# Performance work log

Hardware: AMD Instinct MI355X
Metric: run time of the kernel (lower is better)

Reference implementation:

```python
import jax, jax.numpy as jnp
import numpy as np

N, E, G = 20000, 320000, 32


def setup_inputs() -> dict:
    key = jax.random.key(0)
    ks = list(jax.random.split(key, 16))
    def nrm(i, shape, s):
        return jax.random.normal(ks[i], shape, jnp.float32) * s
    inp = {}
    inp['x'] = nrm(0, (N, 768), 1.0)
    inp['edge_index'] = jax.random.randint(ks[1], (2, E), 0, N)
    inp['batch'] = jnp.sort(jax.random.randint(ks[2], (N,), 0, G))
    # xavier-ish scales
    inp['proj_w'] = nrm(3, (768, 768), 0.036); inp['proj_b'] = jnp.zeros((768,), jnp.float32)
    inp['gat1_w'] = nrm(4, (768, 1024), 0.033)
    inp['att1_src'] = nrm(5, (4, 256), 0.06); inp['att1_dst'] = nrm(6, (4, 256), 0.06)
    inp['gat1_b'] = jnp.zeros((1024,), jnp.float32)
    inp['ln1_g'] = jnp.ones((1024,), jnp.float32); inp['ln1_b'] = jnp.zeros((1024,), jnp.float32)
    inp['gat2_w'] = nrm(7, (1024, 1024), 0.031)
    inp['att2_src'] = nrm(8, (4, 256), 0.06); inp['att2_dst'] = nrm(9, (4, 256), 0.06)
    inp['gat2_b'] = jnp.zeros((1024,), jnp.float32)
    inp['ln2_g'] = jnp.ones((1024,), jnp.float32); inp['ln2_b'] = jnp.zeros((1024,), jnp.float32)
    inp['gat3_w'] = nrm(10, (1024, 256), 0.04)
    inp['att3_src'] = nrm(11, (1, 256), 0.08); inp['att3_dst'] = nrm(12, (1, 256), 0.08)
    inp['gat3_b'] = jnp.zeros((256,), jnp.float32)
    inp['ln3_g'] = jnp.ones((256,), jnp.float32); inp['ln3_b'] = jnp.zeros((256,), jnp.float32)
    inp['cls1_w'] = nrm(13, (768, 128), 0.047); inp['cls1_b'] = jnp.zeros((128,), jnp.float32)
    inp['cls2_w'] = nrm(14, (128, 1), 0.12); inp['cls2_b'] = jnp.zeros((1,), jnp.float32)
    return inp


def layer_norm(x, g, b, eps=1e-5):
    mu = x.mean(-1, keepdims=True)
    v = ((x - mu) ** 2).mean(-1, keepdims=True)
    return (x - mu) * jax.lax.rsqrt(v + eps) * g + b


def gat_conv(x, src, dst, W, a_src, a_dst, bias, concat):
    # PyG GATConv (eval mode): linear -> per-head additive attention ->
    # segment softmax over incoming edges of each dst node -> scatter-sum.
    n = x.shape[0]
    H, C = a_src.shape
    h = (x @ W).reshape(n, H, C)                      # [N,H,C]
    e_s = (h * a_src[None]).sum(-1)                   # [N,H]
    e_d = (h * a_dst[None]).sum(-1)                   # [N,H]
    logits = jax.nn.leaky_relu(e_s[src] + e_d[dst], 0.2)   # [Etot,H]
    m = jax.ops.segment_max(logits, dst, num_segments=n)   # self-loops -> no empty segments
    ex = jnp.exp(logits - m[dst])
    den = jax.ops.segment_sum(ex, dst, num_segments=n)
    alpha = ex / (den[dst] + 1e-16)                   # [Etot,H]
    out = jax.ops.segment_sum(h[src] * alpha[:, :, None], dst, num_segments=n)  # [N,H,C]
    out = out.reshape(n, H * C) if concat else out.mean(axis=1)
    return out + bias


def reference(x, edge_index, batch, proj_w, proj_b,
              gat1_w, att1_src, att1_dst, gat1_b, ln1_g, ln1_b,
              gat2_w, att2_src, att2_dst, gat2_b, ln2_g, ln2_b,
              gat3_w, att3_src, att3_dst, gat3_b, ln3_g, ln3_b,
              cls1_w, cls1_b, cls2_w, cls2_b):
    n = x.shape[0]
    loop = jnp.arange(n)
    src = jnp.concatenate([edge_index[0], loop])  # GATConv adds self-loops
    dst = jnp.concatenate([edge_index[1], loop])
    h = jax.nn.elu(x @ proj_w + proj_b)
    x1 = jax.nn.elu(layer_norm(gat_conv(h, src, dst, gat1_w, att1_src, att1_dst, gat1_b, True), ln1_g, ln1_b))
    x2 = jax.nn.elu(layer_norm(gat_conv(x1, src, dst, gat2_w, att2_src, att2_dst, gat2_b, True), ln2_g, ln2_b)) + x1
    x3 = jax.nn.elu(layer_norm(gat_conv(x2, src, dst, gat3_w, att3_src, att3_dst, gat3_b, False), ln3_g, ln3_b))
    cnt = jax.ops.segment_sum(jnp.ones((n, 1), x3.dtype), batch, num_segments=G)
    s = jax.ops.segment_sum(x3, batch, num_segments=G)
    mean = s / jnp.maximum(cnt, 1.0)
    mx = jax.ops.segment_max(x3, batch, num_segments=G)
    pooled = jnp.concatenate([mean, mx, s], axis=1)   # [G, 3*256]
    out = jax.nn.relu(pooled @ cls1_w + cls1_b) @ cls2_w + cls2_b
    return out.reshape(-1)
```

## Files before the change

### kernel.cpp

```cpp
#include <hip/hip_runtime.h>
#include <math.h>

typedef float floatx4 __attribute__((ext_vector_type(4)));
typedef _Float16 f16x8 __attribute__((ext_vector_type(8)));
typedef _Float16 f16x4 __attribute__((ext_vector_type(4)));

template<int N> struct f16vec_t;
template<> struct f16vec_t<4> { typedef f16x4 type; };
template<> struct f16vec_t<8> { typedef f16x8 type; };

__device__ __forceinline__ unsigned encf(float f) {
    unsigned u = __float_as_uint(f);
    return (u & 0x80000000u) ? ~u : (u | 0x80000000u);
}
__device__ __forceinline__ float decf(unsigned u) {
    u = (u & 0x80000000u) ? (u & 0x7FFFFFFFu) : ~u;
    return __uint_as_float(u);
}
__device__ __forceinline__ void glds16(const void* g, void* l) {
    __builtin_amdgcn_global_load_lds(
        (const __attribute__((address_space(1))) unsigned int*)g,
        (__attribute__((address_space(3))) unsigned int*)l, 16, 0, 0);
}

__global__ __launch_bounds__(256) void cvt_f16_kernel(
    const float* __restrict__ in, _Float16* __restrict__ out, size_t n4)
{
    size_t i = (size_t)blockIdx.x * 256 + threadIdx.x;
    if (i >= n4) return;
    float4 v = ((const float4*)in)[i];
    f16x4 o;
    o[0] = (_Float16)v.x; o[1] = (_Float16)v.y; o[2] = (_Float16)v.z; o[3] = (_Float16)v.w;
    ((f16x4*)out)[i] = o;
}

__global__ __launch_bounds__(256) void wt_kernel(
    const float* __restrict__ w, _Float16* __restrict__ wt, int K, int N)
{
    __shared__ float t[32][33];
    int bx = blockIdx.x * 32, by = blockIdx.y * 32;
    int tx = threadIdx.x & 31, ty = threadIdx.x >> 5;
    for (int r = ty; r < 32; r += 8)
        t[r][tx] = w[(size_t)(by + r) * N + bx + tx];
    __syncthreads();
    for (int r = ty; r < 32; r += 8)
        wt[(size_t)(bx + r) * K + by + tx] = (_Float16)t[tx][r];
}

__global__ __launch_bounds__(256) void gemm_f16(
    const _Float16* __restrict__ A, const _Float16* __restrict__ BT,
    const float* __restrict__ bias, _Float16* __restrict__ C,
    int M, int K, int N, int act)
{
    __shared__ _Float16 Al[2][128 * 32];
    __shared__ _Float16 Bl[2][128 * 32];
    int tid = threadIdx.x;
    int lane = tid & 63, wave = tid >> 6;
    int row0 = blockIdx.y * 128, col0 = blockIdx.x * 128;
    int wm = (wave >> 1) * 64, wn = (wave & 1) * 64;
    int l15 = lane & 15, quad = lane >> 4;

    int rg0 = wave * 2, rg1 = rg0 + 1;
    int srow0 = rg0 * 16 + (lane >> 2);
    int srow1 = rg1 * 16 + (lane >> 2);
    int scol = (lane & 3) * 8;
    int arow0 = row0 + srow0; if (arow0 > M - 1) arow0 = M - 1;
    int arow1 = row0 + srow1; if (arow1 > M - 1) arow1 = M - 1;
    const _Float16* gA0 = A + (size_t)arow0 * K + scol;
    const _Float16* gA1 = A + (size_t)arow1 * K + scol;
    const _Float16* gB0 = BT + (size_t)(col0 + srow0) * K + scol;
    const _Float16* gB1 = BT + (size_t)(col0 + srow1) * K + scol;

    floatx4 acc[4][4] = {};

    glds16(gA0, &Al[0][rg0 * 512]);
    glds16(gA1, &Al[0][rg1 * 512]);
    glds16(gB0, &Bl[0][rg0 * 512]);
    glds16(gB1, &Bl[0][rg1 * 512]);

    int nk = K >> 5;
    for (int it = 0; it < nk; it++) {
        int cur = it & 1, nxt = cur ^ 1;
        __syncthreads();
        if (it + 1 < nk) {
            int k1 = (it + 1) << 5;
            glds16(gA0 + k1, &Al[nxt][rg0 * 512]);
            glds16(gA1 + k1, &Al[nxt][rg1 * 512]);
            glds16(gB0 + k1, &Bl[nxt][rg0 * 512]);
            glds16(gB1 + k1, &Bl[nxt][rg1 * 512]);
        }
        f16x8 af[4], bfr[4];
        #pragma unroll
        for (int i = 0; i < 4; i++) {
            af[i]  = *(const f16x8*)&Al[cur][(wm + i * 16 + l15) * 32 + quad * 8];
            bfr[i] = *(const f16x8*)&Bl[cur][(wn + i * 16 + l15) * 32 + quad * 8];
        }
        #pragma unroll
        for (int i = 0; i < 4; i++)
            #pragma unroll
            for (int j = 0; j < 4; j++)
                acc[i][j] = __builtin_amdgcn_mfma_f32_16x16x32_f16(af[i], bfr[j], acc[i][j], 0, 0, 0);
    }

    #pragma unroll
    for (int i = 0; i < 4; i++) {
        #pragma unroll
        for (int v = 0; v < 4; v++) {
            int gr = row0 + wm + i * 16 + quad * 4 + v;
            if (gr >= M) continue;
            #pragma unroll
            for (int j = 0; j < 4; j++) {
                int gc = col0 + wn + j * 16 + l15;
                float val = acc[i][j][v];
                if (bias) val += bias[gc];
                if (act) val = val > 0.f ? val : (expf(val) - 1.f);
                C[(size_t)gr * N + gc] = (_Float16)val;
            }
        }
    }
}

__global__ __launch_bounds__(256) void attn_scores_kernel(
    const _Float16* __restrict__ h, const float* __restrict__ asrc, const float* __restrict__ adst,
    float* __restrict__ es, float* __restrict__ ed, int Nn, int H)
{
    int wid = (blockIdx.x * 256 + threadIdx.x) >> 6;
    int lane = threadIdx.x & 63;
    if (wid >= Nn * H) return;
    int node = wid / H, hh = wid % H;
    const _Float16* hp = h + (size_t)node * H * 256 + hh * 256 + lane * 4;
    f16x4 v = *(const f16x4*)hp;
    float ss = 0.f, sd = 0.f;
    #pragma unroll
    for (int j = 0; j < 4; j++) {
        float f = (float)v[j];
        ss = fmaf(f, asrc[hh * 256 + lane * 4 + j], ss);
        sd = fmaf(f, adst[hh * 256 + lane * 4 + j], sd);
    }
    #pragma unroll
    for (int o = 32; o; o >>= 1) { ss += __shfl_down(ss, o); sd += __shfl_down(sd, o); }
    if (lane == 0) { es[wid] = ss; ed[wid] = sd; }
}

__global__ __launch_bounds__(256) void csr_init(int* __restrict__ deg, int Nn) {
    int i = blockIdx.x * 256 + threadIdx.x;
    if (i < Nn) deg[i] = 1;
}
__global__ __launch_bounds__(256) void csr_count(const int* __restrict__ ei, int* __restrict__ deg, int E) {
    int i = blockIdx.x * 256 + threadIdx.x;
    if (i < E) atomicAdd(&deg[ei[E + i]], 1);
}
__global__ __launch_bounds__(256) void scan1(const int* __restrict__ deg, int* __restrict__ incl,
                                             int* __restrict__ bsums, int Nn) {
    __shared__ int sd[256];
    int idx = blockIdx.x * 256 + threadIdx.x;
    sd[threadIdx.x] = (idx < Nn) ? deg[idx] : 0;
    __syncthreads();
    for (int o = 1; o < 256; o <<= 1) {
        int x = (threadIdx.x >= (unsigned)o) ? sd[threadIdx.x - o] : 0;
        __syncthreads();
        sd[threadIdx.x] += x;
        __syncthreads();
    }
    if (idx < Nn) incl[idx] = sd[threadIdx.x];
    if (threadIdx.x == 255) bsums[blockIdx.x] = sd[255];
}
__global__ void scan2(int* __restrict__ bsums, int nb) {
    if (blockIdx.x == 0 && threadIdx.x == 0) {
        int run = 0;
        for (int i = 0; i < nb; i++) { int v = bsums[i]; bsums[i] = run; run += v; }
    }
}
__global__ __launch_bounds__(256) void scan3(const int* __restrict__ incl, const int* __restrict__ deg,
                                             const int* __restrict__ bsums, int* __restrict__ rowstart,
                                             int* __restrict__ cursor, int Nn) {
    int idx = blockIdx.x * 256 + threadIdx.x;
    if (idx >= Nn) return;
    int rs = incl[idx] - deg[idx] + bsums[blockIdx.x];
    rowstart[idx] = rs;
    cursor[idx] = rs;
}
__global__ __launch_bounds__(256) void csr_fill(const int* __restrict__ ei, int* __restrict__ cursor,
                                                int* __restrict__ csrc, int E, int Nn) {
    int i = blockIdx.x * 256 + threadIdx.x;
    if (i >= E + Nn) return;
    int s, d;
    if (i < E) { s = ei[i]; d = ei[E + i]; } else { s = d = i - E; }
    int pos = atomicAdd(&cursor[d], 1);
    csrc[pos] = s;
}

template<int H>
__global__ __launch_bounds__(256) void seg_softmax(
    const int* __restrict__ rowstart, const int* __restrict__ deg,
    const int* __restrict__ csrc, const float* __restrict__ es,
    const float* __restrict__ ed, float* __restrict__ wse, int Nn)
{
    int d = (blockIdx.x * 256 + threadIdx.x) >> 6;
    int lane = threadIdx.x & 63;
    if (d >= Nn) return;
    constexpr int S = 64 / H;
    int head = lane & (H - 1);
    int slot = lane / H;
    int st = rowstart[d], dg = deg[d];
    float edv = ed[d * H + head];
    float m = -1e30f;
    for (int j = slot; j < dg; j += S) {
        float l = es[csrc[st + j] * H + head] + edv;
        l = l > 0.f ? l : 0.2f * l;
        wse[(size_t)(st + j) * H + head] = l;
        m = fmaxf(m, l);
    }
    #pragma unroll
    for (int o = H; o < 64; o <<= 1) m = fmaxf(m, __shfl_xor(m, o));
    float z = 0.f;
    for (int j = slot; j < dg; j += S) {
        float e = expf(wse[(size_t)(st + j) * H + head] - m);
        wse[(size_t)(st + j) * H + head] = e;
        z += e;
    }
    #pragma unroll
    for (int o = H; o < 64; o <<= 1) z += __shfl_xor(z, o);
    float rz = 1.f / (z + 1e-16f);
    for (int j = slot; j < dg; j += S)
        wse[(size_t)(st + j) * H + head] *= rz;
}

template<int H>
__global__ __launch_bounds__(H == 4 ? 128 : 64) void gat_gather_ln(
    const int* __restrict__ rowstart, const int* __restrict__ deg,
    const int* __restrict__ csrc, const float* __restrict__ wse,
    const _Float16* __restrict__ h,
    const float* __restrict__ bias, const float* __restrict__ gam,
    const float* __restrict__ bet, const float* resid,
    float* xout, _Float16* xout16)
{
    constexpr int T = (H == 4) ? 128 : 64;
    constexpr int CPT = (H == 4) ? 8 : 4;
    constexpr int NW = T / 64;
    constexpr int HC = H * 256;
    typedef typename f16vec_t<CPT>::type hvec;
    int d = blockIdx.x;
    int t = threadIdx.x;
    int lane = t & 63, wave = t >> 6;
    int ch0 = t * CPT;
    int head2 = ch0 >> 8;
    int st = rowstart[d], dg = deg[d];
    const _Float16* hb = h + ch0;

    float acc[CPT];
    #pragma unroll
    for (int k = 0; k < CPT; k++) acc[k] = 0.f;

    int j = 0;
    for (; j + 2 <= dg; j += 2) {
        int s0 = csrc[st + j], s1 = csrc[st + j + 1];
        float w0 = wse[(size_t)(st + j) * H + head2];
        float w1 = wse[(size_t)(st + j + 1) * H + head2];
        hvec v0 = *(const hvec*)(hb + (size_t)s0 * HC);
        hvec v1 = *(const hvec*)(hb + (size_t)s1 * HC);
        #pragma unroll
        for (int k = 0; k < CPT; k++)
            acc[k] += w0 * (float)v0[k] + w1 * (float)v1[k];
    }
    if (j < dg) {
        int s0 = csrc[st + j];
        float w0 = wse[(size_t)(st + j) * H + head2];
        hvec v0 = *(const hvec*)(hb + (size_t)s0 * HC);
        #pragma unroll
        for (int k = 0; k < CPT; k++) acc[k] += w0 * (float)v0[k];
    }

    #pragma unroll
    for (int k = 0; k < CPT; k++) acc[k] += bias[ch0 + k];

    __shared__ float sm[NW > 1 ? NW : 1];
    float sum = 0.f;
    #pragma unroll
    for (int k = 0; k < CPT; k++) sum += acc[k];
    #pragma unroll
    for (int o = 32; o; o >>= 1) sum += __shfl_down(sum, o);
    float tot;
    if (NW > 1) {
        if (lane == 0) sm[wave] = sum;
        __syncthreads();
        tot = 0.f;
        #pragma unroll
        for (int w2 = 0; w2 < NW; w2++) tot += sm[w2];
    } else {
        tot = __shfl(sum, 0);
    }
    float mean = tot / (float)HC;
    float sq = 0.f;
    #pragma unroll
    for (int k = 0; k < CPT; k++) { float dd = acc[k] - mean; sq = fmaf(dd, dd, sq); }
    #pragma unroll
    for (int o = 32; o; o >>= 1) sq += __shfl_down(sq, o);
    if (NW > 1) {
        __syncthreads();
        if (lane == 0) sm[wave] = sq;
        __syncthreads();
        tot = 0.f;
        #pragma unroll
        for (int w2 = 0; w2 < NW; w2++) tot += sm[w2];
    } else {
        tot = __shfl(sq, 0);
    }
    float rstd = rsqrtf(tot / (float)HC + 1e-5f);

    float y[CPT];
    #pragma unroll
    for (int k = 0; k < CPT; k++) {
        float v = (acc[k] - mean) * rstd * gam[ch0 + k] + bet[ch0 + k];
        y[k] = v > 0.f ? v : (expf(v) - 1.f);
    }
    if (resid) {
        #pragma unroll
        for (int q = 0; q < CPT / 4; q++) {
            float4 r = ((const float4*)resid)[(size_t)d * (HC / 4) + t * (CPT / 4) + q];
            y[q * 4 + 0] += r.x; y[q * 4 + 1] += r.y; y[q * 4 + 2] += r.z; y[q * 4 + 3] += r.w;
        }
    }
    #pragma unroll
    for (int q = 0; q < CPT / 4; q++)
        ((float4*)xout)[(size_t)d * (HC / 4) + t * (CPT / 4) + q] =
            make_float4(y[q * 4 + 0], y[q * 4 + 1], y[q * 4 + 2], y[q * 4 + 3]);
    if (xout16) {
        hvec o;
        #pragma unroll
        for (int k = 0; k < CPT; k++) o[k] = (_Float16)y[k];
        *(hvec*)(xout16 + (size_t)d * HC + ch0) = o;
    }
}

__global__ __launch_bounds__(256) void pool_kernel(
    const float* __restrict__ x3, const int* __restrict__ batch,
    float* __restrict__ ps, unsigned* __restrict__ pm, int* __restrict__ cnt, int Nn)
{
    int c = threadIdx.x;
    int n0 = blockIdx.x * 16;
    int end = n0 + 16; if (end > Nn) end = Nn;
    if (n0 >= Nn) return;
    int curg = batch[n0];
    float s = 0.f, m = -1e30f; int k = 0;
    for (int n = n0; n < end; n++) {
        int g = batch[n];
        if (g != curg) {
            atomicAdd(&ps[curg * 256 + c], s);
            atomicMax(&pm[curg * 256 + c], encf(m));
            if (c == 0) atomicAdd(&cnt[curg], k);
            s = 0.f; m = -1e30f; k = 0; curg = g;
        }
        float v = x3[(size_t)n * 256 + c];
        s += v; m = fmaxf(m, v); k++;
    }
    atomicAdd(&ps[curg * 256 + c], s);
    atomicMax(&pm[curg * 256 + c], encf(m));
    if (c == 0) atomicAdd(&cnt[curg], k);
}

__global__ __launch_bounds__(128) void classifier_kernel(
    const float* __restrict__ ps, const unsigned* __restrict__ pm, const int* __restrict__ cnt,
    const float* __restrict__ w1, const float* __restrict__ b1,
    const float* __restrict__ w2, const float* __restrict__ b2, float* __restrict__ out)
{
    int g = blockIdx.x;
    int tid = threadIdx.x;
    __shared__ float pooled[768];
    __shared__ float red[2];
    float c = (float)cnt[g];
    if (c < 1.f) c = 1.f;
    for (int i = tid; i < 256; i += 128) {
        float s = ps[g * 256 + i];
        pooled[i] = s / c;
        pooled[256 + i] = decf(pm[g * 256 + i]);
        pooled[512 + i] = s;
    }
    __syncthreads();
    float acc = b1[tid];
    for (int k = 0; k < 768; k++) acc = fmaf(pooled[k], w1[k * 128 + tid], acc);
    acc = fmaxf(acc, 0.f);
    float v = acc * w2[tid];
    #pragma unroll
    for (int o = 32; o; o >>= 1) v += __shfl_down(v, o);
    if ((tid & 63) == 0) red[tid >> 6] = v;
    __syncthreads();
    if (tid == 0) out[g] = red[0] + red[1] + b2[0];
}

extern "C" void kernel_launch(void* const* d_in, const int* in_sizes, int n_in,
                              void* d_out, int out_size, void* d_ws, size_t ws_size,
                              hipStream_t stream)
{
    const float* x      = (const float*)d_in[0];
    const int*   ei     = (const int*)d_in[1];
    const int*   batch  = (const int*)d_in[2];
    const float* proj_w = (const float*)d_in[3];
    const float* proj_b = (const float*)d_in[4];
    const float* gat1_w = (const float*)d_in[5];
    const float* att1_s = (const float*)d_in[6];
    const float* att1_d = (const float*)d_in[7];
    const float* gat1_b = (const float*)d_in[8];
    const float* ln1_g  = (const float*)d_in[9];
    const float* ln1_b  = (const float*)d_in[10];
    const float* gat2_w = (const float*)d_in[11];
    const float* att2_s = (const float*)d_in[12];
    const float* att2_d = (const float*)d_in[13];
    const float* gat2_b = (const float*)d_in[14];
    const float* ln2_g  = (const float*)d_in[15];
    const float* ln2_b  = (const float*)d_in[16];
    const float* gat3_w = (const float*)d_in[17];
    const float* att3_s = (const float*)d_in[18];
    const float* att3_d = (const float*)d_in[19];
    const float* gat3_b = (const float*)d_in[20];
    const float* ln3_g  = (const float*)d_in[21];
    const float* ln3_b  = (const float*)d_in[22];
    const float* cls1_w = (const float*)d_in[23];
    const float* cls1_b = (const float*)d_in[24];
    const float* cls2_w = (const float*)d_in[25];
    const float* cls2_b = (const float*)d_in[26];

    int Nn = in_sizes[0] / 768;
    int E  = in_sizes[1] / 2;
    int Gg = out_size;
    int Etot = E + Nn;
    int nb  = (Nn + 255) / 256;

    char* w = (char*)d_ws;
    size_t off = 0;
    auto alloc = [&](size_t bytes) -> char* {
        char* r = w + off;
        off += (bytes + 255) & ~(size_t)255;
        return r;
    };
    size_t NB16 = (size_t)Nn * 1024 * sizeof(_Float16);
    size_t NB32 = (size_t)Nn * 1024 * sizeof(float);
    _Float16* P = (_Float16*)alloc(NB16);
    _Float16* Q = (_Float16*)alloc(NB16);
    float*  X = (float*)alloc(NB32);
    _Float16* projT = (_Float16*)alloc((size_t)768 * 768 * 2);
    _Float16* g1T   = (_Float16*)alloc((size_t)1024 * 768 * 2);
    _Float16* g2T   = (_Float16*)alloc((size_t)1024 * 1024 * 2);
    _Float16* g3T   = (_Float16*)alloc((size_t)256 * 1024 * 2);
    float*    es    = (float*)alloc((size_t)Nn * 4 * 4);
    float*    ed_   = (float*)alloc((size_t)Nn * 4 * 4);
    int*      deg   = (int*)alloc((size_t)Nn * 4);
    int*      incl  = (int*)alloc((size_t)Nn * 4);
    int*      rowst = (int*)alloc((size_t)Nn * 4);
    int*      curs  = (int*)alloc((size_t)Nn * 4);
    int*      bsums = (int*)alloc((size_t)nb * 4);
    int*      csrc  = (int*)alloc((size_t)Etot * 4);
    float*    wse   = (float*)alloc((size_t)Etot * 4 * 4);
    float*    ps    = (float*)alloc((size_t)Gg * 256 * 4);
    unsigned* pm    = (unsigned*)alloc((size_t)Gg * 256 * 4);
    int*      cnt   = (int*)alloc(256);

    dim3 blk(256);

    wt_kernel<<<dim3(768 / 32, 768 / 32), blk, 0, stream>>>(proj_w, projT, 768, 768);
    wt_kernel<<<dim3(1024 / 32, 768 / 32), blk, 0, stream>>>(gat1_w, g1T, 768, 1024);
    wt_kernel<<<dim3(1024 / 32, 1024 / 32), blk, 0, stream>>>(gat2_w, g2T, 1024, 1024);
    wt_kernel<<<dim3(256 / 32, 1024 / 32), blk, 0, stream>>>(gat3_w, g3T, 1024, 256);

    {
        size_t n4 = (size_t)Nn * 768 / 4;
        cvt_f16_kernel<<<dim3((unsigned)((n4 + 255) / 256)), blk, 0, stream>>>(x, P, n4);
    }

    csr_init<<<dim3(nb), blk, 0, stream>>>(deg, Nn);
    csr_count<<<dim3((E + 255) / 256), blk, 0, stream>>>(ei, deg, E);
    scan1<<<dim3(nb), blk, 0, stream>>>(deg, incl, bsums, Nn);
    scan2<<<dim3(1), dim3(64), 0, stream>>>(bsums, nb);
    scan3<<<dim3(nb), blk, 0, stream>>>(incl, deg, bsums, rowst, curs, Nn);
    csr_fill<<<dim3((Etot + 255) / 256), blk, 0, stream>>>(ei, curs, csrc, E, Nn);

    int mg = (Nn + 127) / 128;

    gemm_f16<<<dim3(768 / 128, mg), blk, 0, stream>>>(P, projT, proj_b, Q, Nn, 768, 768, 1);

    auto run_gat = [&](const _Float16* xin16, const _Float16* WT, const float* as_, const float* ad_,
                       const float* gb, const float* lg, const float* lb, const float* resid,
                       _Float16* hbuf, float* xout, _Float16* xout16,
                       int K, int H, int C) {
        int HC = H * C;
        gemm_f16<<<dim3(HC / 128, mg), blk, 0, stream>>>(xin16, WT, nullptr, hbuf, Nn, K, HC, 0);
        int nw = Nn * H;
        attn_scores_kernel<<<dim3((nw + 3) / 4), blk, 0, stream>>>(hbuf, as_, ad_, es, ed_, Nn, H);
        if (H == 4) {
            seg_softmax<4><<<dim3((Nn + 3) / 4), blk, 0, stream>>>(rowst, deg, csrc, es, ed_, wse, Nn);
            gat_gather_ln<4><<<dim3(Nn), dim3(128), 0, stream>>>(rowst, deg, csrc, wse, hbuf,
                                                                 gb, lg, lb, resid, xout, xout16);
        } else {
            seg_softmax<1><<<dim3((Nn + 3) / 4), blk, 0, stream>>>(rowst, deg, csrc, es, ed_, wse, Nn);
            gat_gather_ln<1><<<dim3(Nn), dim3(64), 0, stream>>>(rowst, deg, csrc, wse, hbuf,
                                                                gb, lg, lb, resid, xout, xout16);
        }
    };

    run_gat(Q, g1T, att1_s, att1_d, gat1_b, ln1_g, ln1_b, nullptr, P, X, Q, 768, 4, 256);
    run_gat(Q, g2T, att2_s, att2_d, gat2_b, ln2_g, ln2_b, X, P, X, Q, 1024, 4, 256);
    run_gat(Q, g3T, att3_s, att3_d, gat3_b, ln3_g, ln3_b, nullptr, P, X, nullptr, 1024, 1, 256);

    hipMemsetAsync(ps, 0, (size_t)Gg * 256 * 4, stream);
    hipMemsetAsync(pm, 0, (size_t)Gg * 256 * 4, stream);
    hipMemsetAsync(cnt, 0, (size_t)Gg * 4, stream);
    pool_kernel<<<dim3((Nn + 15) / 16), blk, 0, stream>>>(X, batch, ps, pm, cnt, Nn);
    classifier_kernel<<<dim3(Gg), dim3(128), 0, stream>>>(ps, pm, cnt, cls1_w, cls1_b, cls2_w, cls2_b, (float*)d_out);
}
```

Before: 807.1 us.

## Merge weight transposes into one launch, use fast exp, unroll gather by four

```diff
diff --git a/kernel.cpp b/kernel.cpp
--- a/kernel.cpp
+++ b/kernel.cpp
@@ -17,6 +17,7 @@
     u = (u & 0x80000000u) ? (u & 0x7FFFFFFFu) : ~u;
     return __uint_as_float(u);
 }
+__device__ __forceinline__ float fexp(float x) { return __expf(x); }
 __device__ __forceinline__ void glds16(const void* g, void* l) {
     __builtin_amdgcn_global_load_lds(
         (const __attribute__((address_space(1))) unsigned int*)g,
@@ -34,11 +35,21 @@
     ((f16x4*)out)[i] = o;
 }
 
-__global__ __launch_bounds__(256) void wt_kernel(
-    const float* __restrict__ w, _Float16* __restrict__ wt, int K, int N)
-{
+__global__ __launch_bounds__(256) void wt_all_kernel(
+    const float* __restrict__ w0, _Float16* __restrict__ o0,
+    const float* __restrict__ w1, _Float16* __restrict__ o1,
+    const float* __restrict__ w2, _Float16* __restrict__ o2,
+    const float* __restrict__ w3, _Float16* __restrict__ o3)
+{
+    int b = blockIdx.x;
+    const float* w; _Float16* wt; int K, N, lb;
+    if (b < 576)       { w = w0; wt = o0; K = 768;  N = 768;  lb = b; }
+    else if (b < 1344) { w = w1; wt = o1; K = 768;  N = 1024; lb = b - 576; }
+    else if (b < 2368) { w = w2; wt = o2; K = 1024; N = 1024; lb = b - 1344; }
+    else               { w = w3; wt = o3; K = 1024; N = 256;  lb = b - 2368; }
+    int ntx = N / 32;
+    int bx = (lb % ntx) * 32, by = (lb / ntx) * 32;
     __shared__ float t[32][33];
-    int bx = blockIdx.x * 32, by = blockIdx.y * 32;
     int tx = threadIdx.x & 31, ty = threadIdx.x >> 5;
     for (int r = ty; r < 32; r += 8)
         t[r][tx] = w[(size_t)(by + r) * N + bx + tx];
@@ -113,7 +124,7 @@
                 int gc = col0 + wn + j * 16 + l15;
                 float val = acc[i][j][v];
                 if (bias) val += bias[gc];
-                if (act) val = val > 0.f ? val : (expf(val) - 1.f);
+                if (act) val = val > 0.f ? val : (fexp(val) - 1.f);
                 C[(size_t)gr * N + gc] = (_Float16)val;
             }
         }
@@ -215,7 +226,7 @@
     for (int o = H; o < 64; o <<= 1) m = fmaxf(m, __shfl_xor(m, o));
     float z = 0.f;
     for (int j = slot; j < dg; j += S) {
-        float e = expf(wse[(size_t)(st + j) * H + head] - m);
+        float e = fexp(wse[(size_t)(st + j) * H + head] - m);
         wse[(size_t)(st + j) * H + head] = e;
         z += e;
     }
@@ -253,17 +264,23 @@
     for (int k = 0; k < CPT; k++) acc[k] = 0.f;
 
     int j = 0;
-    for (; j + 2 <= dg; j += 2) {
+    for (; j + 4 <= dg; j += 4) {
         int s0 = csrc[st + j], s1 = csrc[st + j + 1];
+        int s2 = csrc[st + j + 2], s3 = csrc[st + j + 3];
         float w0 = wse[(size_t)(st + j) * H + head2];
         float w1 = wse[(size_t)(st + j + 1) * H + head2];
+        float w2 = wse[(size_t)(st + j + 2) * H + head2];
+        float w3 = wse[(size_t)(st + j + 3) * H + head2];
         hvec v0 = *(const hvec*)(hb + (size_t)s0 * HC);
         hvec v1 = *(const hvec*)(hb + (size_t)s1 * HC);
+        hvec v2 = *(const hvec*)(hb + (size_t)s2 * HC);
+        hvec v3 = *(const hvec*)(hb + (size_t)s3 * HC);
         #pragma unroll
         for (int k = 0; k < CPT; k++)
-            acc[k] += w0 * (float)v0[k] + w1 * (float)v1[k];
-    }
-    if (j < dg) {
+            acc[k] += w0 * (float)v0[k] + w1 * (float)v1[k]
+                    + w2 * (float)v2[k] + w3 * (float)v3[k];
+    }
+    for (; j < dg; j++) {
         int s0 = csrc[st + j];
         float w0 = wse[(size_t)(st + j) * H + head2];
         hvec v0 = *(const hvec*)(hb + (size_t)s0 * HC);
@@ -312,7 +329,7 @@
     #pragma unroll
     for (int k = 0; k < CPT; k++) {
         float v = (acc[k] - mean) * rstd * gam[ch0 + k] + bet[ch0 + k];
-        y[k] = v > 0.f ? v : (expf(v) - 1.f);
+        y[k] = v > 0.f ? v : (fexp(v) - 1.f);
     }
     if (resid) {
         #pragma unroll
@@ -457,10 +474,8 @@
 
     dim3 blk(256);
 
-    wt_kernel<<<dim3(768 / 32, 768 / 32), blk, 0, stream>>>(proj_w, projT, 768, 768);
-    wt_kernel<<<dim3(1024 / 32, 768 / 32), blk, 0, stream>>>(gat1_w, g1T, 768, 1024);
-    wt_kernel<<<dim3(1024 / 32, 1024 / 32), blk, 0, stream>>>(gat2_w, g2T, 1024, 1024);
-    wt_kernel<<<dim3(256 / 32, 1024 / 32), blk, 0, stream>>>(gat3_w, g3T, 1024, 256);
+    wt_all_kernel<<<dim3(2624), blk, 0, stream>>>(proj_w, projT, gat1_w, g1T,
+                                                  gat2_w, g2T, gat3_w, g3T);
 
     {
         size_t n4 = (size_t)Nn * 768 / 4;
```

Result: faster. 783.9 us (-2.9%).
